# Kernel tuning notes

Measured on AMD Instinct MI355X. Metric: run time of the kernel, lower is better.

The kernel has to match this reference:

```python
import jax, jax.numpy as jnp
import numpy as np

ALPHA = 3.0
TOP_K = 16
N_NODES = 8192
EMB_DIM = 128


def setup_inputs() -> dict:
    key = jax.random.key(0)
    k1, k2, k3, k4, k5, k6 = jax.random.split(key, 6)
    return {
        "idx": jnp.arange(N_NODES, dtype=jnp.int64 if jax.config.jax_enable_x64 else jnp.int32),
        "emb1_w": jax.random.normal(k1, (N_NODES, EMB_DIM), dtype=jnp.float32),
        "emb2_w": jax.random.normal(k2, (N_NODES, EMB_DIM), dtype=jnp.float32),
        "th1_w": jax.random.normal(k3, (EMB_DIM, EMB_DIM), dtype=jnp.float32) * 0.08,
        "th1_b": jax.random.normal(k4, (EMB_DIM,), dtype=jnp.float32) * 0.02,
        "th2_w": jax.random.normal(k5, (EMB_DIM, EMB_DIM), dtype=jnp.float32) * 0.08,
        "th2_b": jax.random.normal(k6, (EMB_DIM,), dtype=jnp.float32) * 0.02,
    }


def reference(idx, emb1_w, emb2_w, th1_w, th1_b, th2_w, th2_b):
    # embedding lookup + linear + tanh (nn.Linear: x @ W.T + b)
    e1 = jnp.tanh(ALPHA * (emb1_w[idx] @ th1_w.T + th1_b))  # [N, D]
    e2 = jnp.tanh(ALPHA * (emb2_w[idx] @ th2_w.T + th2_b))  # [N, D]
    # antisymmetric score -> tanh -> relu  => [N, N]
    adj = jax.nn.relu(jnp.tanh(ALPHA * (e1 @ e2.T - e2 @ e1.T)))
    # eval-mode top-k per row, scatter a binary mask (s1.fill_(1) in the source)
    _, t1 = jax.lax.top_k(adj, TOP_K)  # [N, k]
    n = idx.shape[0]
    rows = jnp.arange(n)[:, None]
    mask = jnp.zeros((n, n), dtype=adj.dtype).at[rows, t1].set(1.0)
    return adj * mask
```

## Files before the change

kernel.cpp:

```cpp
#include <hip/hip_runtime.h>

#define NN    8192
#define DD    128
#define TOPK  16

#define CUT_D 7.99881172180175781
#define CUT_F 7.99881172180175781f
#define EPS_F 2.0e-2f
#define MAXSUS 512


__global__ __launch_bounds__(256) void k1ws(
    const int* __restrict__ idx,
    const float* __restrict__ emb1, const float* __restrict__ W1, const float* __restrict__ b1,
    const float* __restrict__ emb2, const float* __restrict__ W2, const float* __restrict__ b2,
    float* __restrict__ e1ws, float* __restrict__ e2ws)
{
    const float* emb; const float* W; const float* bias; float* eo;
    if (blockIdx.y == 0) { emb = emb1; W = W1; bias = b1; eo = e1ws; }
    else                 { emb = emb2; W = W2; bias = b2; eo = e2ws; }

    __shared__ float Wl[128][65];
    __shared__ float Xl[16][65];
    __shared__ int rowi[16];

    int t  = threadIdx.x;
    int r0 = blockIdx.x * 16;
    if (t < 16) {
        bool wide = (idx[1] == 0 && idx[2] == 1);
        int row = wide ? idx[2 * (r0 + t)] : idx[r0 + t];
        rowi[t] = min(max(row, 0), NN - 1);
    }
    __syncthreads();

    int d = t & 127, rh = t >> 7;
    double acc[8];
    #pragma unroll
    for (int q = 0; q < 8; q++) acc[q] = 0.0;

    for (int h = 0; h < 2; h++) {
        if (h) __syncthreads();
        for (int i = t; i < 128 * 64; i += 256)
            Wl[i >> 6][i & 63] = W[(i >> 6) * DD + h * 64 + (i & 63)];
        for (int i = t; i < 16 * 64; i += 256)
            Xl[i >> 6][i & 63] = emb[(size_t)rowi[i >> 6] * DD + h * 64 + (i & 63)];
        __syncthreads();
        for (int k = 0; k < 64; k++) {
            double wv = (double)Wl[d][k];
            #pragma unroll
            for (int q = 0; q < 8; q++) acc[q] += (double)Xl[rh + 2 * q][k] * wv;
        }
    }
    double bv = (double)bias[d];
    #pragma unroll
    for (int q = 0; q < 8; q++)
        eo[(size_t)(r0 + rh + 2 * q) * DD + d] = (float)tanh(3.0 * (acc[q] + bv));
}

__global__ __launch_bounds__(256) void ksel32(
    const float* __restrict__ e1, const float* __restrict__ e2,
    float* __restrict__ out)
{
    __shared__ union {
        struct { float A1[32][36], A2[32][36], B1[32][132], B2[32][132]; } p;
        float vals[NN];
    } sm;
    __shared__ unsigned char cls[32][128];
    __shared__ int idxs[32][TOPK];
    __shared__ unsigned int suspects[MAXSUS];
    __shared__ unsigned int nsus;
    __shared__ int fb[32];
    __shared__ int anyfb;
    __shared__ float redv[256];
    __shared__ int   redi[256];
    __shared__ unsigned int si[TOPK];
    __shared__ float sv[TOPK];

    int ti = blockIdx.x;
    int t  = threadIdx.x;
    int rx = t & 31, ry = t >> 5;
    int mc0 = rx * 4, mr0 = ry * 4;

    if (t == 0) { nsus = 0; anyfb = 0; }

    float acc[4][4];
    #pragma unroll
    for (int r = 0; r < 4; r++)
        #pragma unroll
        for (int c = 0; c < 4; c++) acc[r][c] = 0.f;

    for (int h = 0; h < 4; h++) {
        __syncthreads();
        {
            int rr = t >> 3, dq = t & 7;
            int o  = h * 32 + dq * 4;
            float4 va1 = *(const float4*)&e1[(size_t)(ti * 32 + rr) * DD + o];
            float4 va2 = *(const float4*)&e2[(size_t)(ti * 32 + rr) * DD + o];
            int dd = dq * 4;
            sm.p.A1[dd+0][rr] = va1.x; sm.p.A1[dd+1][rr] = va1.y;
            sm.p.A1[dd+2][rr] = va1.z; sm.p.A1[dd+3][rr] = va1.w;
            sm.p.A2[dd+0][rr] = va2.x; sm.p.A2[dd+1][rr] = va2.y;
            sm.p.A2[dd+2][rr] = va2.z; sm.p.A2[dd+3][rr] = va2.w;
        }
        #pragma unroll
        for (int it2 = 0; it2 < 4; it2++) {
            int id = it2 * 256 + t;
            int rr = id >> 3, dq = id & 7;
            int o  = h * 32 + dq * 4;
            float4 vb1 = *(const float4*)&e1[(size_t)rr * DD + o];
            float4 vb2 = *(const float4*)&e2[(size_t)rr * DD + o];
            int dd = dq * 4;
            sm.p.B1[dd+0][rr] = vb1.x; sm.p.B1[dd+1][rr] = vb1.y;
            sm.p.B1[dd+2][rr] = vb1.z; sm.p.B1[dd+3][rr] = vb1.w;
            sm.p.B2[dd+0][rr] = vb2.x; sm.p.B2[dd+1][rr] = vb2.y;
            sm.p.B2[dd+2][rr] = vb2.z; sm.p.B2[dd+3][rr] = vb2.w;
        }
        __syncthreads();

        #pragma unroll 4
        for (int d = 0; d < 32; d++) {
            float4 a1 = *(const float4*)&sm.p.A1[d][mr0];
            float4 a2 = *(const float4*)&sm.p.A2[d][mr0];
            float4 b1 = *(const float4*)&sm.p.B1[d][mc0];
            float4 b2 = *(const float4*)&sm.p.B2[d][mc0];
            float a1v[4] = {a1.x, a1.y, a1.z, a1.w};
            float a2v[4] = {a2.x, a2.y, a2.z, a2.w};
            float b1v[4] = {b1.x, b1.y, b1.z, b1.w};
            float b2v[4] = {b2.x, b2.y, b2.z, b2.w};
            #pragma unroll
            for (int r = 0; r < 4; r++)
                #pragma unroll
                for (int c = 0; c < 4; c++) {
                    acc[r][c] = fmaf(a1v[r],  b2v[c], acc[r][c]);
                    acc[r][c] = fmaf(-a2v[r], b1v[c], acc[r][c]);
                }
        }
    }

    #pragma unroll
    for (int r = 0; r < 4; r++)
        #pragma unroll
        for (int c = 0; c < 4; c++) {
            float del = 3.0f * acc[r][c] - CUT_F;
            cls[mr0 + r][mc0 + c] = (del > 0.f) ? 1 : 0;
            if (fabsf(del) < EPS_F) {
                unsigned int slot = atomicAdd(&nsus, 1u);
                if (slot < MAXSUS)
                    suspects[slot] = ((unsigned int)(mr0 + r) << 8) | (unsigned int)(mc0 + c);
            }
        }
    __syncthreads();

    {
        unsigned int n = nsus < MAXSUS ? nsus : MAXSUS;
        for (unsigned int s = t; s < n; s += 256) {
            int r = (int)(suspects[s] >> 8), c = (int)(suspects[s] & 255u);
            size_t grow = (size_t)(ti * 32 + r) * DD;
            size_t gcol = (size_t)c * DD;
            double d1 = 0.0, d2 = 0.0;
            for (int k = 0; k < DD; k++) {
                d1 = fma((double)e1[grow + k], (double)e2[gcol + k], d1);
                d2 = fma((double)e2[grow + k], (double)e1[gcol + k], d2);
            }
            cls[r][c] = (3.0 * (d1 - d2) >= CUT_D) ? 1 : 0;
        }
    }
    for (int i = t; i < 32 * TOPK; i += 256) idxs[i >> 4][i & 15] = -1;
    __syncthreads();

    int wv = t >> 6, lane = t & 63;
    for (int rr = 0; rr < 8; rr++) {
        int rloc = wv * 8 + rr;
        unsigned long long w0 = __ballot(cls[rloc][lane] != 0);
        unsigned long long w1 = __ballot(cls[rloc][64 + lane] != 0);
        if (lane == 0) {
            bool ok = (__popcll(w0) + __popcll(w1) >= TOPK) &&
                      !(nsus > MAXSUS);
            if (ok) {
                int rank = 0;
                unsigned long long x = w0; int base = 0;
                while (x && rank < TOPK) {
                    int b = __ffsll(x) - 1;
                    idxs[rloc][rank] = base + b;
                    x &= x - 1; rank++;
                }
                x = w1; base = 64;
                while (x && rank < TOPK) {
                    int b = __ffsll(x) - 1;
                    idxs[rloc][rank] = base + b;
                    x &= x - 1; rank++;
                }
                fb[rloc] = 0;
            } else {
                fb[rloc] = 1;
                anyfb = 1;
                #pragma unroll
                for (int s = 0; s < TOPK; s++) idxs[rloc][s] = -1;
            }
        }
    }
    __syncthreads();

    for (int i = t; i < 32 * TOPK; i += 256) {
        int r = i >> 4, col = idxs[r][i & 15];
        if (col >= 0)
            out[(size_t)(ti * 32 + r) * NN + col] = 1.0f;
    }

    if (!anyfb) return;
    __syncthreads();

    for (int q = 0; q < 32; q++) {
        if (!fb[q]) continue;
        int row = ti * 32 + q;
        for (int j = t; j < NN; j += 256) {
            double d1 = 0.0, d2 = 0.0;
            for (int k = 0; k < 128; k++) {
                double r1k = (double)e1[(size_t)row * DD + k];
                double r2k = (double)e2[(size_t)row * DD + k];
                d1 = fma(r1k, (double)e2[(size_t)j * DD + k], d1);
                d2 = fma(r2k, (double)e1[(size_t)j * DD + k], d2);
            }
            double arg = 3.0 * (d1 - d2);
            float v = (arg >= CUT_D) ? 1.0f : (float)tanh(arg);
            sm.vals[j] = v > 0.f ? v : 0.f;
        }
        __syncthreads();
        for (int s = 0; s < TOPK; s++) {
            float bv = -1.f; int bj = 1 << 30;
            for (int j = t; j < NN; j += 256) {
                float v = sm.vals[j];
                if (v > bv || (v == bv && j < bj)) { bv = v; bj = j; }
            }
            redv[t] = bv; redi[t] = bj;
            __syncthreads();
            for (int sft = 128; sft > 0; sft >>= 1) {
                if (t < sft) {
                    if (redv[t + sft] > redv[t] ||
                        (redv[t + sft] == redv[t] && redi[t + sft] < redi[t])) {
                        redv[t] = redv[t + sft];
                        redi[t] = redi[t + sft];
                    }
                }
                __syncthreads();
            }
            if (t == 0) {
                si[s] = (unsigned int)redi[0];
                sv[s] = redv[0];
                sm.vals[redi[0]] = -2.f;
            }
            __syncthreads();
        }
        if (t < TOPK)
            out[(size_t)row * NN + si[t]] = sv[t];
        __syncthreads();
    }
}

#define OFF_VAL    16
#define OFF_E1     2112
#define OFF_E2     2240

__global__ __launch_bounds__(256) void k1_fb(
    const int* __restrict__ idx,
    const float* __restrict__ emb1, const float* __restrict__ W1, const float* __restrict__ b1,
    const float* __restrict__ emb2, const float* __restrict__ W2, const float* __restrict__ b2,
    float* out)
{
    const float* emb; const float* W; const float* bias; int eoff;
    if (blockIdx.y == 0) { emb = emb1; W = W1; bias = b1; eoff = OFF_E1; }
    else                 { emb = emb2; W = W2; bias = b2; eoff = OFF_E2; }

    __shared__ float Wl[128][65];
    __shared__ float Xl[16][65];
    __shared__ int rowi[16];

    int t  = threadIdx.x;
    int r0 = blockIdx.x * 16;
    if (t < 16) {
        bool wide = (idx[1] == 0 && idx[2] == 1);
        int row = wide ? idx[2 * (r0 + t)] : idx[r0 + t];
        rowi[t] = min(max(row, 0), NN - 1);
    }
    __syncthreads();

    int d = t & 127, rh = t >> 7;
    double acc[8];
    #pragma unroll
    for (int q = 0; q < 8; q++) acc[q] = 0.0;

    for (int h = 0; h < 2; h++) {
        if (h) __syncthreads();
        for (int i = t; i < 128 * 64; i += 256)
            Wl[i >> 6][i & 63] = W[(i >> 6) * DD + h * 64 + (i & 63)];
        for (int i = t; i < 16 * 64; i += 256)
            Xl[i >> 6][i & 63] = emb[(size_t)rowi[i >> 6] * DD + h * 64 + (i & 63)];
        __syncthreads();
        for (int k = 0; k < 64; k++) {
            double wv = (double)Wl[d][k];
            #pragma unroll
            for (int q = 0; q < 8; q++) acc[q] += (double)Xl[rh + 2 * q][k] * wv;
        }
    }
    double bv = (double)bias[d];
    #pragma unroll
    for (int q = 0; q < 8; q++)
        out[(size_t)(r0 + rh + 2 * q) * NN + eoff + d] = (float)tanh(3.0 * (acc[q] + bv));
}

__global__ __launch_bounds__(256) void k2sel_fb(float* out)
{
    int ti = blockIdx.x;
    __shared__ float A1[32][68], A2[32][68], B1[32][68], B2[32][68];
    __shared__ unsigned char cls[64][128];
    __shared__ int fb[64];
    __shared__ float vals[NN];
    __shared__ float redv[256];
    __shared__ int   redi[256];

    int t  = threadIdx.x;
    int tx = t & 15, ty = t >> 4;
    int mr0 = ty * 4, mc0 = tx * 4;

    for (int tjj = 0; tjj < 2; tjj++) {
        double acc[4][4];
        #pragma unroll
        for (int r = 0; r < 4; r++)
            #pragma unroll
            for (int c = 0; c < 4; c++) acc[r][c] = 0.0;

        for (int h = 0; h < 4; h++) {
            __syncthreads();
            #pragma unroll
            for (int it2 = 0; it2 < 2; it2++) {
                int idx2 = it2 * 256 + t;
                int rr = idx2 >> 3, dq = idx2 & 7;
                int o  = h * 32 + dq * 4;
                size_t rbA = (size_t)(ti * 64 + rr) * NN;
                size_t rbB = (size_t)(tjj * 64 + rr) * NN;
                float4 v1 = *(const float4*)&out[rbA + OFF_E1 + o];
                float4 v2 = *(const float4*)&out[rbA + OFF_E2 + o];
                float4 v3 = *(const float4*)&out[rbB + OFF_E1 + o];
                float4 v4 = *(const float4*)&out[rbB + OFF_E2 + o];
                int dd = dq * 4;
                A1[dd+0][rr] = v1.x; A1[dd+1][rr] = v1.y; A1[dd+2][rr] = v1.z; A1[dd+3][rr] = v1.w;
                A2[dd+0][rr] = v2.x; A2[dd+1][rr] = v2.y; A2[dd+2][rr] = v2.z; A2[dd+3][rr] = v2.w;
                B1[dd+0][rr] = v3.x; B1[dd+1][rr] = v3.y; B1[dd+2][rr] = v3.z; B1[dd+3][rr] = v3.w;
                B2[dd+0][rr] = v4.x; B2[dd+1][rr] = v4.y; B2[dd+2][rr] = v4.z; B2[dd+3][rr] = v4.w;
            }
            __syncthreads();
            #pragma unroll 2
            for (int d = 0; d < 32; d++) {
                double a1v[4], a2v[4], b1v[4], b2v[4];
                #pragma unroll
                for (int r = 0; r < 4; r++) {
                    a1v[r] = (double)A1[d][mr0 + r];
                    a2v[r] = (double)A2[d][mr0 + r];
                }
                #pragma unroll
                for (int c = 0; c < 4; c++) {
                    b1v[c] = (double)B1[d][mc0 + c];
                    b2v[c] = (double)B2[d][mc0 + c];
                }
                #pragma unroll
                for (int r = 0; r < 4; r++)
                    #pragma unroll
                    for (int c = 0; c < 4; c++) {
                        acc[r][c] = fma(a1v[r],  b2v[c], acc[r][c]);
                        acc[r][c] = fma(-a2v[r], b1v[c], acc[r][c]);
                    }
            }
        }
        #pragma unroll
        for (int r = 0; r < 4; r++)
            #pragma unroll
            for (int c = 0; c < 4; c++)
                cls[mr0 + r][tjj * 64 + mc0 + c] = (3.0 * acc[r][c] >= CUT_D) ? 1 : 0;
    }
    __syncthreads();

    int wv = t >> 6, lane = t & 63;
    unsigned int* ou = (unsigned int*)out;
    for (int rr = 0; rr < 16; rr++) {
        int rloc = wv * 16 + rr;
        unsigned long long w0 = __ballot(cls[rloc][lane] != 0);
        unsigned long long w1 = __ballot(cls[rloc][64 + lane] != 0);
        if (lane == 0) {
            size_t rb = (size_t)(ti * 64 + rloc) * NN;
            if (__popcll(w0) + __popcll(w1) >= TOPK) {
                int rank = 0;
                unsigned long long x = w0; int base = 0;
                while (x && rank < TOPK) {
                    int b = __ffsll(x) - 1;
                    ou[rb + rank] = (unsigned int)(base + b);
                    out[rb + OFF_VAL + rank] = 1.0f;
                    x &= x - 1; rank++;
                }
                x = w1; base = 64;
                while (x && rank < TOPK) {
                    int b = __ffsll(x) - 1;
                    ou[rb + rank] = (unsigned int)(base + b);
                    out[rb + OFF_VAL + rank] = 1.0f;
                    x &= x - 1; rank++;
                }
                fb[rloc] = 0;
            } else fb[rloc] = 1;
        }
    }
    __syncthreads();

    for (int q = 0; q < 64; q++) {
        if (!fb[q]) continue;
        int row = ti * 64 + q;
        size_t rb = (size_t)row * NN;
        const float* r1 = &out[rb + OFF_E1];
        const float* r2 = &out[rb + OFF_E2];
        for (int j = t; j < NN; j += 256) {
            const float* e1j = &out[(size_t)j * NN + OFF_E1];
            const float* e2j = &out[(size_t)j * NN + OFF_E2];
            double d1 = 0.0, d2 = 0.0;
            for (int k = 0; k < 128; k++) {
                d1 = fma((double)r1[k], (double)e2j[k], d1);
                d2 = fma((double)r2[k], (double)e1j[k], d2);
            }
            double arg = 3.0 * (d1 - d2);
            float v = (arg >= CUT_D) ? 1.0f : (float)tanh(arg);
            vals[j] = v > 0.f ? v : 0.f;
        }
        __syncthreads();
        for (int s = 0; s < TOPK; s++) {
            float bv = -1.f; int bj = 1 << 30;
            for (int j = t; j < NN; j += 256) {
                float v = vals[j];
                if (v > bv || (v == bv && j < bj)) { bv = v; bj = j; }
            }
            redv[t] = bv; redi[t] = bj;
            __syncthreads();
            for (int sft = 128; sft > 0; sft >>= 1) {
                if (t < sft) {
                    if (redv[t + sft] > redv[t] ||
                        (redv[t + sft] == redv[t] && redi[t + sft] < redi[t])) {
                        redv[t] = redv[t + sft];
                        redi[t] = redi[t + sft];
                    }
                }
                __syncthreads();
            }
            if (t == 0) {
                ou[rb + s]            = (unsigned int)redi[0];
                out[rb + OFF_VAL + s] = redv[0];
                vals[redi[0]] = -2.f;
            }
            __syncthreads();
        }
        __syncthreads();
    }
}

__global__ __launch_bounds__(256) void k5_fb(float* out)
{
    __shared__ unsigned int si[TOPK];
    __shared__ float sv[TOPK];
    int t = threadIdx.x;
    size_t rb = (size_t)blockIdx.x * NN;
    if (t < TOPK) {
        si[t] = ((const unsigned int*)out)[rb + t];
        sv[t] = out[rb + OFF_VAL + t];
    }
    __syncthreads();

    unsigned int li[TOPK]; float lv[TOPK];
    #pragma unroll
    for (int s = 0; s < TOPK; s++) { li[s] = si[s]; lv[s] = sv[s]; }

    #pragma unroll
    for (int it2 = 0; it2 < 8; it2++) {
        unsigned int w = it2 * 256 + t;
        float4 v = make_float4(0.f, 0.f, 0.f, 0.f);
        #pragma unroll
        for (int s = 0; s < TOPK; s++) {
            unsigned int j = li[s];
            if ((j >> 2) == w) ((float*)&v)[j & 3] = lv[s];
        }
        *(float4*)&out[rb + (size_t)w * 4] = v;
    }
}

extern "C" void kernel_launch(void* const* d_in, const int* in_sizes, int n_in,
                              void* d_out, int out_size, void* d_ws, size_t ws_size,
                              hipStream_t stream)
{
    (void)in_sizes; (void)n_in; (void)out_size;

    const int*   idx  = (const int*)  d_in[0];
    const float* emb1 = (const float*)d_in[1];
    const float* emb2 = (const float*)d_in[2];
    const float* th1w = (const float*)d_in[3];
    const float* th1b = (const float*)d_in[4];
    const float* th2w = (const float*)d_in[5];
    const float* th2b = (const float*)d_in[6];
    float* out = (float*)d_out;

    const size_t need = 2ull * NN * DD * sizeof(float);
    if (d_ws != nullptr && ws_size >= need) {
        float* e1ws = (float*)d_ws;
        float* e2ws = e1ws + (size_t)NN * DD;
        hipMemsetAsync(out, 0, (size_t)NN * NN * sizeof(float), stream);
        k1ws  <<<dim3(NN / 16, 2), 256, 0, stream>>>(idx, emb1, th1w, th1b,
                                                     emb2, th2w, th2b, e1ws, e2ws);
        ksel32<<<NN / 32,          256, 0, stream>>>(e1ws, e2ws, out);
    } else {
        k1_fb   <<<dim3(NN / 16, 2), 256, 0, stream>>>(idx, emb1, th1w, th1b,
                                                       emb2, th2w, th2b, out);
        k2sel_fb<<<NN / 64,          256, 0, stream>>>(out);
        k5_fb   <<<NN,               256, 0, stream>>>(out);
    }
}
```

Before: 119.2 us.

## Replace output memset and scatter with header buffer plus single fill kernel

The selection kernel now writes per-row top-k indices and values into a compact workspace header instead of scattering into a pre-zeroed output. A new fill kernel writes each output row once with vectorized float4 stores, inserting the selected values, which removes the separate full-matrix memset pass. This adds an extra kernel launch and requires additional workspace for the header.

```diff
diff --git a/kernel.cpp b/kernel.cpp
--- a/kernel.cpp
+++ b/kernel.cpp
@@ -57,9 +57,9 @@
         eo[(size_t)(r0 + rh + 2 * q) * DD + d] = (float)tanh(3.0 * (acc[q] + bv));
 }
 
-__global__ __launch_bounds__(256) void ksel32(
+__global__ __launch_bounds__(256) void ksel32h(
     const float* __restrict__ e1, const float* __restrict__ e2,
-    float* __restrict__ out)
+    unsigned int* __restrict__ hdr)
 {
     __shared__ union {
         struct { float A1[32][36], A2[32][36], B1[32][132], B2[32][132]; } p;
@@ -165,7 +165,7 @@
             cls[r][c] = (3.0 * (d1 - d2) >= CUT_D) ? 1 : 0;
         }
     }
-    for (int i = t; i < 32 * TOPK; i += 256) idxs[i >> 4][i & 15] = -1;
+    for (int i = t; i < 32 * TOPK; i += 256) idxs[i >> 4][i & 15] = 0;
     __syncthreads();
 
     int wv = t >> 6, lane = t & 63;
@@ -174,8 +174,7 @@
         unsigned long long w0 = __ballot(cls[rloc][lane] != 0);
         unsigned long long w1 = __ballot(cls[rloc][64 + lane] != 0);
         if (lane == 0) {
-            bool ok = (__popcll(w0) + __popcll(w1) >= TOPK) &&
-                      !(nsus > MAXSUS);
+            bool ok = (__popcll(w0) + __popcll(w1) >= TOPK) && !(nsus > MAXSUS);
             if (ok) {
                 int rank = 0;
                 unsigned long long x = w0; int base = 0;
@@ -194,17 +193,16 @@
             } else {
                 fb[rloc] = 1;
                 anyfb = 1;
-                #pragma unroll
-                for (int s = 0; s < TOPK; s++) idxs[rloc][s] = -1;
-            }
-        }
-    }
-    __syncthreads();
-
-    for (int i = t; i < 32 * TOPK; i += 256) {
-        int r = i >> 4, col = idxs[r][i & 15];
-        if (col >= 0)
-            out[(size_t)(ti * 32 + r) * NN + col] = 1.0f;
+            }
+        }
+    }
+    __syncthreads();
+
+    for (int i = t; i < 32 * 32; i += 256) {
+        int r = i >> 5, w = i & 31;
+        unsigned int val = (w < TOPK) ? (unsigned int)idxs[r][w]
+                                      : __float_as_uint(1.0f);
+        hdr[(size_t)(ti * 32 + r) * 32 + w] = val;
     }
 
     if (!anyfb) return;
@@ -251,9 +249,42 @@
             }
             __syncthreads();
         }
-        if (t < TOPK)
-            out[(size_t)row * NN + si[t]] = sv[t];
-        __syncthreads();
+        if (t < TOPK) {
+            hdr[(size_t)row * 32 + t]        = si[t];
+            hdr[(size_t)row * 32 + TOPK + t] = __float_as_uint(sv[t]);
+        }
+        __syncthreads();
+    }
+}
+
+__global__ __launch_bounds__(256) void kfill(
+    const unsigned int* __restrict__ hdr, float* __restrict__ out)
+{
+    __shared__ unsigned int si[TOPK];
+    __shared__ float sv[TOPK];
+    int t = threadIdx.x;
+    size_t row = blockIdx.x;
+    if (t < TOPK) {
+        si[t] = hdr[row * 32 + t];
+        sv[t] = __uint_as_float(hdr[row * 32 + TOPK + t]);
+    }
+    __syncthreads();
+
+    unsigned int li[TOPK]; float lv[TOPK];
+    #pragma unroll
+    for (int s = 0; s < TOPK; s++) { li[s] = si[s]; lv[s] = sv[s]; }
+
+    size_t rb = row * NN;
+    #pragma unroll
+    for (int it2 = 0; it2 < 8; it2++) {
+        unsigned int w = it2 * 256 + t;
+        float4 v = make_float4(0.f, 0.f, 0.f, 0.f);
+        #pragma unroll
+        for (int s = 0; s < TOPK; s++) {
+            unsigned int j = li[s];
+            if ((j >> 2) == w) ((float*)&v)[j & 3] = lv[s];
+        }
+        *(float4*)&out[rb + (size_t)w * 4] = v;
     }
 }
 
@@ -501,14 +532,16 @@
     const float* th2b = (const float*)d_in[6];
     float* out = (float*)d_out;
 
-    const size_t need = 2ull * NN * DD * sizeof(float);
-    if (d_ws != nullptr && ws_size >= need) {
+    const size_t eBytes   = 2ull * NN * DD * sizeof(float);
+    const size_t hdrBytes = (size_t)NN * 32 * sizeof(unsigned);
+    if (d_ws != nullptr && ws_size >= eBytes + hdrBytes) {
         float* e1ws = (float*)d_ws;
         float* e2ws = e1ws + (size_t)NN * DD;
-        hipMemsetAsync(out, 0, (size_t)NN * NN * sizeof(float), stream);
-        k1ws  <<<dim3(NN / 16, 2), 256, 0, stream>>>(idx, emb1, th1w, th1b,
-                                                     emb2, th2w, th2b, e1ws, e2ws);
-        ksel32<<<NN / 32,          256, 0, stream>>>(e1ws, e2ws, out);
+        unsigned int* hdr = (unsigned int*)(e2ws + (size_t)NN * DD);
+        k1ws   <<<dim3(NN / 16, 2), 256, 0, stream>>>(idx, emb1, th1w, th1b,
+                                                      emb2, th2w, th2b, e1ws, e2ws);
+        ksel32h<<<NN / 32,          256, 0, stream>>>(e1ws, e2ws, hdr);
+        kfill  <<<NN,               256, 0, stream>>>(hdr, out);
     } else {
         k1_fb   <<<dim3(NN / 16, 2), 256, 0, stream>>>(idx, emb1, th1w, th1b,
                                                        emb2, th2w, th2b, out);
```

Result: slower. 137.8 us (+15.6%).
